# Performance work log

Measured on AMD Instinct MI355X. Metric: run time of the kernel, lower is better.

Reference implementation:

```python
import jax, jax.numpy as jnp
import numpy as np

N_NODES = 100000
N_EDGES = 1200000
D_IN = 16
D_EDGE = 4
H = 64


def setup_inputs() -> dict:
    key = jax.random.key(0)
    ks = jax.random.split(key, 20)
    s = 0.05
    inp = {
        "src": jax.random.randint(ks[0], (N_EDGES,), 0, N_NODES),
        "dst": jax.random.randint(ks[1], (N_EDGES,), 0, N_NODES),
        "t": jax.random.uniform(ks[2], (N_EDGES,), dtype=jnp.float32),
        "x": jax.random.normal(ks[3], (N_NODES, D_IN), dtype=jnp.float32),
        "edge_attr": jax.random.normal(ks[4], (N_EDGES, D_EDGE), dtype=jnp.float32),
        # x_encoder
        "Wx": jax.random.normal(ks[5], (D_IN, H), dtype=jnp.float32) * s,
        "bx": jnp.zeros((H,), dtype=jnp.float32),
        # TransformerConv (heads=1, concat=False)
        "Wq": jax.random.normal(ks[6], (H, H), dtype=jnp.float32) * s,
        "bq": jnp.zeros((H,), dtype=jnp.float32),
        "Wk": jax.random.normal(ks[7], (H, H), dtype=jnp.float32) * s,
        "bk": jnp.zeros((H,), dtype=jnp.float32),
        "Wv": jax.random.normal(ks[8], (H, H), dtype=jnp.float32) * s,
        "bv": jnp.zeros((H,), dtype=jnp.float32),
        "We": jax.random.normal(ks[9], (D_EDGE, H), dtype=jnp.float32) * s,  # lin_edge, bias=False
        "Ws": jax.random.normal(ks[10], (H, H), dtype=jnp.float32) * s,  # lin_skip (root weight)
        "bs": jnp.zeros((H,), dtype=jnp.float32),
        # MLP head
        "W1": jax.random.normal(ks[11], (H, 8), dtype=jnp.float32) * s,
        "b1": jnp.zeros((8,), dtype=jnp.float32),
        "W2": jax.random.normal(ks[12], (8, 1), dtype=jnp.float32) * s,
        "b2": jnp.zeros((1,), dtype=jnp.float32),
    }
    return inp


def reference(src, dst, t, x, edge_attr, Wx, bx, Wq, bq, Wk, bk, Wv, bv, We, Ws, bs, W1, b1, W2, b2):
    # eval mode: dropouts are identity; TGN memory.update_state is a pure
    # side effect and does not influence the returned output.
    xe = x @ Wx + bx                             # [N, H]

    # TransformerConv, heads=1, concat=False, flow src -> dst
    q = xe @ Wq + bq                             # [N, H]
    k = xe @ Wk + bk                             # [N, H]
    v = xe @ Wv + bv                             # [N, H]
    e = edge_attr @ We                           # [E, H]

    k_e = k[src] + e                             # [E, H]
    v_e = v[src] + e                             # [E, H]
    alpha = jnp.sum(q[dst] * k_e, axis=-1) / jnp.sqrt(jnp.float32(H))  # [E]

    # softmax over incoming edges per destination node
    m = jax.ops.segment_max(alpha, dst, num_segments=N_NODES)
    a = jnp.exp(alpha - m[dst])
    denom = jax.ops.segment_sum(a, dst, num_segments=N_NODES)
    w = a / (denom[dst] + 1e-16)                 # [E]

    agg = jax.ops.segment_sum(v_e * w[:, None], dst, num_segments=N_NODES)  # [N, H]
    h_local = agg + (xe @ Ws + bs)               # root/skip connection

    h = h_local[dst]                             # [E, H]
    h = jax.nn.relu(h @ W1 + b1)                 # [E, 8]
    out = (h @ W2 + b2)[:, 0]                    # [E]
    return out
```

## Files before the change

kernel.cpp:

```cpp
#include <hip/hip_runtime.h>

#define H 64
#define CAP 48

typedef int nint4 __attribute__((ext_vector_type(4)));

#define OFF_M   0
#define OFF_U   256
#define OFF_W   272
#define OFF_C   288
#define OFF_R   292
#define OFF_R0  356
#define OFF_PV  360
#define OFF_PE  488
#define OFF_PS  520
#define OFF_BH1 648
#define OFF_BH2 656
#define CST_N   664

__device__ __forceinline__ unsigned f2bf(float f) {
    unsigned u = __float_as_uint(f);
    u += 0x7fffu + ((u >> 16) & 1u);
    return u >> 16;
}
__device__ __forceinline__ float bf_lo(unsigned u) { return __uint_as_float(u << 16); }
__device__ __forceinline__ float bf_hi(unsigned u) { return __uint_as_float(u & 0xffff0000u); }

struct Params {
    const int* src; const int* dst; const float4* ea4; const float* x;
    const float* Wx; const float* bx;
    const float* Wq; const float* bq;
    const float* Wk; const float* bk;
    const float* Wv; const float* bv;
    const float* We; const float* Ws; const float* bs;
    const float* W1; const float* b1; const float* W2; const float* b2;
    int* cursor; nint4* csr; float* cst; float* g; float* out;
    int N, E;
};

__device__ void do_fold(const Params& P, float* __restrict__ cst)
{
    __shared__ float sWf[4][16][64];
    __shared__ float sbf[4][64];
    const int t = threadIdx.x;
    const int c = t & 63, m = t >> 6;
    const float* W; const float* b;
    switch (m) {
        case 0:  W = P.Wq; b = P.bq; break;
        case 1:  W = P.Wk; b = P.bk; break;
        case 2:  W = P.Wv; b = P.bv; break;
        default: W = P.Ws; b = P.bs; break;
    }
    float acc[16];
#pragma unroll
    for (int i = 0; i < 16; ++i) acc[i] = 0.f;
    float bacc = b[c];
    for (int j = 0; j < 64; ++j) {
        const float wv = W[j * 64 + c];
        bacc += P.bx[j] * wv;
#pragma unroll
        for (int i = 0; i < 16; ++i) acc[i] += P.Wx[i * 64 + j] * wv;
    }
#pragma unroll
    for (int i = 0; i < 16; ++i) sWf[m][i][c] = acc[i];
    sbf[m][c] = bacc;
    __syncthreads();

    {
        const int i = t >> 4, j = t & 15;
        float s = 0.f;
        for (int cc = 0; cc < 64; ++cc) s += sWf[0][i][cc] * sWf[1][j][cc];
        cst[OFF_M + i * 16 + j] = s;
    }
    if (t < 16) {
        float su = 0.f, sw = 0.f;
        for (int cc = 0; cc < 64; ++cc) {
            su += sWf[1][t][cc] * sbf[0][cc];
            sw += sWf[0][t][cc] * sbf[1][cc];
        }
        cst[OFF_U + t] = su;
        cst[OFF_W + t] = sw;
    }
    if (t == 0) {
        float s = 0.f;
        for (int cc = 0; cc < 64; ++cc) s += sbf[0][cc] * sbf[1][cc];
        cst[OFF_C] = s;
    }
    if (t < 64) {
        const int j = t >> 4, i = t & 15;
        float s = 0.f;
        for (int cc = 0; cc < 64; ++cc) s += P.We[j * 64 + cc] * sWf[0][i][cc];
        cst[OFF_R + j * 16 + i] = s;
    }
    if (t < 4) {
        float s = 0.f;
        for (int cc = 0; cc < 64; ++cc) s += P.We[t * 64 + cc] * sbf[0][cc];
        cst[OFF_R0 + t] = s;
    }
    if (t < 128) {
        const int i = t >> 3, j = t & 7;
        float sv = 0.f, ss = 0.f;
        for (int cc = 0; cc < 64; ++cc) {
            const float w1 = P.W1[cc * 8 + j];
            sv += sWf[2][i][cc] * w1;
            ss += sWf[3][i][cc] * w1;
        }
        cst[OFF_PV + i * 8 + j] = sv;
        cst[OFF_PS + i * 8 + j] = ss;
    }
    if (t < 32) {
        const int mm = t >> 3, j = t & 7;
        float s = 0.f;
        for (int cc = 0; cc < 64; ++cc) s += P.We[mm * 64 + cc] * P.W1[cc * 8 + j];
        cst[OFF_PE + mm * 8 + j] = s;
    }
    if (t < 8) {
        float s1 = 0.f, s2 = 0.f;
        for (int cc = 0; cc < 64; ++cc) {
            const float w1 = P.W1[cc * 8 + t];
            s1 += sbf[2][cc] * w1;
            s2 += sbf[3][cc] * w1;
        }
        cst[OFF_BH1 + t] = s1;
        cst[OFF_BH2 + t] = s2 + P.b1[t];
    }
}

__global__ __launch_bounds__(256) void k_fill(Params P)
{
    if (blockIdx.x == 0) {
        do_fold(P, P.cst);
        return;
    }
    const int e = (blockIdx.x - 1) * 256 + threadIdx.x;
    if (e >= P.E) return;
    const int s = P.src[e];
    const int d = P.dst[e];
    const float4 A = P.ea4[e];
    const int pos = atomicAdd(&P.cursor[d], 1);
    if (pos < CAP) {
        nint4 ent;
        ent.x = s;
        ent.y = e;
        ent.z = (int)(f2bf(A.x) | (f2bf(A.y) << 16));
        ent.w = (int)(f2bf(A.z) | (f2bf(A.w) << 16));
        P.csr[(size_t)d * CAP + pos] = ent;
    }
}

__global__ __launch_bounds__(128) void k_agg(Params P)
{
    const int t = threadIdx.x;
    const int l = t & 63;
    const int n = blockIdx.x * 2 + (t >> 6);
    if (n >= P.N) return;
    const int grp = l >> 4;
    const int cg_ = l & 15;
    const float* __restrict__ cst = P.cst;

    const int deg = min(P.cursor[n], CAP);
    const size_t nbase = (size_t)n * CAP;

    const float xd = P.x[(size_t)n * 16 + cg_];

    float y = cst[OFF_U + cg_];
#pragma unroll
    for (int i = 0; i < 16; ++i)
        y += __shfl(xd, i) * cst[OFF_M + i * 16 + cg_];

    float pr0 = cst[OFF_R + 0 * 16 + cg_] * xd;
    float pr1 = cst[OFF_R + 1 * 16 + cg_] * xd;
    float pr2 = cst[OFF_R + 2 * 16 + cg_] * xd;
    float pr3 = cst[OFF_R + 3 * 16 + cg_] * xd;
    float pcd = cst[OFF_W + cg_] * xd;
#pragma unroll
    for (int d = 1; d < 16; d <<= 1) {
        pr0 += __shfl_xor(pr0, d);
        pr1 += __shfl_xor(pr1, d);
        pr2 += __shfl_xor(pr2, d);
        pr3 += __shfl_xor(pr3, d);
        pcd += __shfl_xor(pcd, d);
    }
    const float r0 = pr0 + cst[OFF_R0 + 0];
    const float r1 = pr1 + cst[OFF_R0 + 1];
    const float r2 = pr2 + cst[OFF_R0 + 2];
    const float r3 = pr3 + cst[OFF_R0 + 3];
    const float cd = pcd + cst[OFF_C];

    float T = 0.f, S0 = 0.f, S1 = 0.f, S2 = 0.f, S3 = 0.f, den = 0.f;

    for (int base = 0; base < deg; base += 8) {
        const int ia = base + grp;
        const int ib = base + 4 + grp;
        const bool va = ia < deg;
        const bool vb = ib < deg;
        const nint4 Ea = P.csr[nbase + (va ? ia : 0)];
        const nint4 Eb = P.csr[nbase + (vb ? ib : 0)];
        const float xsa = P.x[(size_t)Ea.x * 16 + cg_];
        const float xsb = P.x[(size_t)Eb.x * 16 + cg_];
        {
            const float A0 = bf_lo((unsigned)Ea.z), A1 = bf_hi((unsigned)Ea.z);
            const float A2 = bf_lo((unsigned)Ea.w), A3 = bf_hi((unsigned)Ea.w);
            float p = y * xsa;
            p += __shfl_xor(p, 1);
            p += __shfl_xor(p, 2);
            p += __shfl_xor(p, 4);
            p += __shfl_xor(p, 8);
            p += cd + A0 * r0 + A1 * r1 + A2 * r2 + A3 * r3;
            const float a = va ? __expf(p * 0.125f) : 0.f;
            T += a * xsa;
            S0 += a * A0; S1 += a * A1; S2 += a * A2; S3 += a * A3;
            den += a;
        }
        {
            const float A0 = bf_lo((unsigned)Eb.z), A1 = bf_hi((unsigned)Eb.z);
            const float A2 = bf_lo((unsigned)Eb.w), A3 = bf_hi((unsigned)Eb.w);
            float p = y * xsb;
            p += __shfl_xor(p, 1);
            p += __shfl_xor(p, 2);
            p += __shfl_xor(p, 4);
            p += __shfl_xor(p, 8);
            p += cd + A0 * r0 + A1 * r1 + A2 * r2 + A3 * r3;
            const float a = vb ? __expf(p * 0.125f) : 0.f;
            T += a * xsb;
            S0 += a * A0; S1 += a * A1; S2 += a * A2; S3 += a * A3;
            den += a;
        }
    }

    T   += __shfl_xor(T, 16);   T   += __shfl_xor(T, 32);
    den += __shfl_xor(den, 16); den += __shfl_xor(den, 32);
    S0  += __shfl_xor(S0, 16);  S0  += __shfl_xor(S0, 32);
    S1  += __shfl_xor(S1, 16);  S1  += __shfl_xor(S1, 32);
    S2  += __shfl_xor(S2, 16);  S2  += __shfl_xor(S2, 32);
    S3  += __shfl_xor(S3, 16);  S3  += __shfl_xor(S3, 32);

    const float inv = 1.f / (den + 1e-16f);
    const float Ti = T * inv;

    float hp[8];
#pragma unroll
    for (int j = 0; j < 8; ++j)
        hp[j] = Ti * cst[OFF_PV + cg_ * 8 + j] + xd * cst[OFF_PS + cg_ * 8 + j];
#pragma unroll
    for (int j = 0; j < 8; ++j) {
        hp[j] += __shfl_xor(hp[j], 1);
        hp[j] += __shfl_xor(hp[j], 2);
        hp[j] += __shfl_xor(hp[j], 4);
        hp[j] += __shfl_xor(hp[j], 8);
    }
    const float dinv = den * inv;
    float val = P.b2[0];
#pragma unroll
    for (int j = 0; j < 8; ++j) {
        const float hid = hp[j]
            + inv * (S0 * cst[OFF_PE + 0 * 8 + j] + S1 * cst[OFF_PE + 1 * 8 + j]
                   + S2 * cst[OFF_PE + 2 * 8 + j] + S3 * cst[OFF_PE + 3 * 8 + j])
            + dinv * cst[OFF_BH1 + j] + cst[OFF_BH2 + j];
        val += fmaxf(hid, 0.f) * P.W2[j];
    }

    if (l == 0) P.g[n] = val;
}

__global__ __launch_bounds__(256) void k_out(
    const int* __restrict__ dst, const float* __restrict__ g,
    float* __restrict__ out, int E)
{
    const int e = blockIdx.x * 256 + threadIdx.x;
    if (e < E) out[e] = g[dst[e]];
}

extern "C" void kernel_launch(void* const* d_in, const int* in_sizes, int n_in,
                              void* d_out, int out_size, void* d_ws, size_t ws_size,
                              hipStream_t stream)
{
    Params P;
    P.src = (const int*)d_in[0];
    P.dst = (const int*)d_in[1];
    P.x   = (const float*)d_in[3];
    P.ea4 = (const float4*)d_in[4];
    P.Wx  = (const float*)d_in[5];
    P.bx  = (const float*)d_in[6];
    P.Wq  = (const float*)d_in[7];
    P.bq  = (const float*)d_in[8];
    P.Wk  = (const float*)d_in[9];
    P.bk  = (const float*)d_in[10];
    P.Wv  = (const float*)d_in[11];
    P.bv  = (const float*)d_in[12];
    P.We  = (const float*)d_in[13];
    P.Ws  = (const float*)d_in[14];
    P.bs  = (const float*)d_in[15];
    P.W1  = (const float*)d_in[16];
    P.b1  = (const float*)d_in[17];
    P.W2  = (const float*)d_in[18];
    P.b2  = (const float*)d_in[19];

    P.E = in_sizes[0];
    P.N = in_sizes[3] / 16;
    P.out = (float*)d_out;

    P.csr    = (nint4*)d_ws;
    P.cursor = (int*)(P.csr + (size_t)P.N * CAP);
    P.cst    = (float*)(P.cursor + P.N);
    P.g      = P.cst + CST_N;

    hipMemsetAsync(P.cursor, 0, (size_t)P.N * sizeof(int), stream);

    const int nbE = (P.E + 255) / 256;
    k_fill<<<nbE + 1, 256, 0, stream>>>(P);
    k_agg<<<(P.N + 1) / 2, 128, 0, stream>>>(P);
    k_out<<<nbE, 256, 0, stream>>>(P.dst, P.g, P.out, P.E);
}
```

Before: 292.0 us.

## Map one node per 16-lane group in aggregation and precompute per-node projections

```diff
diff --git a/kernel.cpp b/kernel.cpp
--- a/kernel.cpp
+++ b/kernel.cpp
@@ -1,6 +1,5 @@
 #include <hip/hip_runtime.h>
 
-#define H 64
 #define CAP 48
 
 typedef int nint4 __attribute__((ext_vector_type(4)));
@@ -34,7 +33,8 @@
     const float* Wv; const float* bv;
     const float* We; const float* Ws; const float* bs;
     const float* W1; const float* b1; const float* W2; const float* b2;
-    int* cursor; nint4* csr; float* cst; float* g; float* out;
+    int* cursor; nint4* csr; float* cst;
+    float* yv; float* rv; float* cdv; float* g; float* out;
     int N, E;
 };
 
@@ -126,25 +126,65 @@
     }
 }
 
+__global__ __launch_bounds__(256) void k_init(Params P)
+{
+    if (blockIdx.x == 0) { do_fold(P, P.cst); return; }
+    const int i = (blockIdx.x - 1) * 256 + threadIdx.x;
+    if (i < P.N) P.cursor[i] = 0;
+}
+
 __global__ __launch_bounds__(256) void k_fill(Params P)
 {
-    if (blockIdx.x == 0) {
-        do_fold(P, P.cst);
+    const int t = threadIdx.x;
+    const int nbE = (P.E + 255) >> 8;
+    if ((int)blockIdx.x < nbE) {
+        const int e = blockIdx.x * 256 + t;
+        if (e >= P.E) return;
+        const int s = P.src[e];
+        const int d = P.dst[e];
+        const float4 A = P.ea4[e];
+        const int pos = atomicAdd(&P.cursor[d], 1);
+        if (pos < CAP) {
+            nint4 ent;
+            ent.x = s;
+            ent.y = e;
+            ent.z = (int)(f2bf(A.x) | (f2bf(A.y) << 16));
+            ent.w = (int)(f2bf(A.z) | (f2bf(A.w) << 16));
+            P.csr[(size_t)d * CAP + pos] = ent;
+        }
         return;
     }
-    const int e = (blockIdx.x - 1) * 256 + threadIdx.x;
-    if (e >= P.E) return;
-    const int s = P.src[e];
-    const int d = P.dst[e];
-    const float4 A = P.ea4[e];
-    const int pos = atomicAdd(&P.cursor[d], 1);
-    if (pos < CAP) {
-        nint4 ent;
-        ent.x = s;
-        ent.y = e;
-        ent.z = (int)(f2bf(A.x) | (f2bf(A.y) << 16));
-        ent.w = (int)(f2bf(A.z) | (f2bf(A.w) << 16));
-        P.csr[(size_t)d * CAP + pos] = ent;
+
+    __shared__ float sx[16][16];
+    const float* __restrict__ cst = P.cst;
+    const int node0 = ((int)blockIdx.x - nbE) * 16;
+    const int nl = t >> 4, cg = t & 15;
+    {
+        const int idx = node0 * 16 + t;
+        sx[nl][cg] = (idx < P.N * 16) ? P.x[idx] : 0.f;
+    }
+    __syncthreads();
+    const int n = node0 + nl;
+    if (n >= P.N) return;
+
+    float y = cst[OFF_U + cg];
+#pragma unroll
+    for (int i = 0; i < 16; ++i)
+        y += sx[nl][i] * cst[OFF_M + i * 16 + cg];
+    P.yv[(size_t)n * 16 + cg] = y;
+
+    if (cg < 4) {
+        float r = cst[OFF_R0 + cg];
+#pragma unroll
+        for (int i = 0; i < 16; ++i)
+            r += cst[OFF_R + cg * 16 + i] * sx[nl][i];
+        P.rv[(size_t)n * 4 + cg] = r;
+    } else if (cg == 4) {
+        float cd = cst[OFF_C];
+#pragma unroll
+        for (int i = 0; i < 16; ++i)
+            cd += cst[OFF_W + i] * sx[nl][i];
+        P.cdv[n] = cd;
     }
 }
 
@@ -152,52 +192,37 @@
 {
     const int t = threadIdx.x;
     const int l = t & 63;
-    const int n = blockIdx.x * 2 + (t >> 6);
-    if (n >= P.N) return;
+    const int wv = t >> 6;
     const int grp = l >> 4;
-    const int cg_ = l & 15;
+    const int cg  = l & 15;
+    const int n   = (blockIdx.x * 2 + wv) * 4 + grp;
     const float* __restrict__ cst = P.cst;
 
-    const int deg = min(P.cursor[n], CAP);
-    const size_t nbase = (size_t)n * CAP;
-
-    const float xd = P.x[(size_t)n * 16 + cg_];
-
-    float y = cst[OFF_U + cg_];
-#pragma unroll
-    for (int i = 0; i < 16; ++i)
-        y += __shfl(xd, i) * cst[OFF_M + i * 16 + cg_];
-
-    float pr0 = cst[OFF_R + 0 * 16 + cg_] * xd;
-    float pr1 = cst[OFF_R + 1 * 16 + cg_] * xd;
-    float pr2 = cst[OFF_R + 2 * 16 + cg_] * xd;
-    float pr3 = cst[OFF_R + 3 * 16 + cg_] * xd;
-    float pcd = cst[OFF_W + cg_] * xd;
-#pragma unroll
-    for (int d = 1; d < 16; d <<= 1) {
-        pr0 += __shfl_xor(pr0, d);
-        pr1 += __shfl_xor(pr1, d);
-        pr2 += __shfl_xor(pr2, d);
-        pr3 += __shfl_xor(pr3, d);
-        pcd += __shfl_xor(pcd, d);
-    }
-    const float r0 = pr0 + cst[OFF_R0 + 0];
-    const float r1 = pr1 + cst[OFF_R0 + 1];
-    const float r2 = pr2 + cst[OFF_R0 + 2];
-    const float r3 = pr3 + cst[OFF_R0 + 3];
-    const float cd = pcd + cst[OFF_C];
+    const bool vn = n < P.N;
+    const int nn = vn ? n : P.N - 1;
+    const int deg = vn ? min(P.cursor[nn], CAP) : 0;
+    const size_t nbase = (size_t)nn * CAP;
+
+    const float xd = P.x[(size_t)nn * 16 + cg];
+    const float y  = P.yv[(size_t)nn * 16 + cg];
+    const float4 rv = *(const float4*)&P.rv[(size_t)nn * 4];
+    const float cd = P.cdv[nn];
+
+    int degM = deg;
+    degM = max(degM, __shfl_xor(degM, 16));
+    degM = max(degM, __shfl_xor(degM, 32));
 
     float T = 0.f, S0 = 0.f, S1 = 0.f, S2 = 0.f, S3 = 0.f, den = 0.f;
 
-    for (int base = 0; base < deg; base += 8) {
-        const int ia = base + grp;
-        const int ib = base + 4 + grp;
-        const bool va = ia < deg;
-        const bool vb = ib < deg;
-        const nint4 Ea = P.csr[nbase + (va ? ia : 0)];
-        const nint4 Eb = P.csr[nbase + (vb ? ib : 0)];
-        const float xsa = P.x[(size_t)Ea.x * 16 + cg_];
-        const float xsb = P.x[(size_t)Eb.x * 16 + cg_];
+    for (int i = 0; i < degM; i += 2) {
+        const bool va = i < deg;
+        const bool vb = (i + 1) < deg;
+        const nint4 Ea = P.csr[nbase + (va ? i : 0)];
+        const nint4 Eb = P.csr[nbase + (vb ? i + 1 : 0)];
+        const int sa = va ? Ea.x : 0;
+        const int sb = vb ? Eb.x : 0;
+        const float xsa = P.x[(size_t)sa * 16 + cg];
+        const float xsb = P.x[(size_t)sb * 16 + cg];
         {
             const float A0 = bf_lo((unsigned)Ea.z), A1 = bf_hi((unsigned)Ea.z);
             const float A2 = bf_lo((unsigned)Ea.w), A3 = bf_hi((unsigned)Ea.w);
@@ -206,7 +231,7 @@
             p += __shfl_xor(p, 2);
             p += __shfl_xor(p, 4);
             p += __shfl_xor(p, 8);
-            p += cd + A0 * r0 + A1 * r1 + A2 * r2 + A3 * r3;
+            p += cd + A0 * rv.x + A1 * rv.y + A2 * rv.z + A3 * rv.w;
             const float a = va ? __expf(p * 0.125f) : 0.f;
             T += a * xsa;
             S0 += a * A0; S1 += a * A1; S2 += a * A2; S3 += a * A3;
@@ -220,7 +245,7 @@
             p += __shfl_xor(p, 2);
             p += __shfl_xor(p, 4);
             p += __shfl_xor(p, 8);
-            p += cd + A0 * r0 + A1 * r1 + A2 * r2 + A3 * r3;
+            p += cd + A0 * rv.x + A1 * rv.y + A2 * rv.z + A3 * rv.w;
             const float a = vb ? __expf(p * 0.125f) : 0.f;
             T += a * xsb;
             S0 += a * A0; S1 += a * A1; S2 += a * A2; S3 += a * A3;
@@ -228,20 +253,13 @@
         }
     }
 
-    T   += __shfl_xor(T, 16);   T   += __shfl_xor(T, 32);
-    den += __shfl_xor(den, 16); den += __shfl_xor(den, 32);
-    S0  += __shfl_xor(S0, 16);  S0  += __shfl_xor(S0, 32);
-    S1  += __shfl_xor(S1, 16);  S1  += __shfl_xor(S1, 32);
-    S2  += __shfl_xor(S2, 16);  S2  += __shfl_xor(S2, 32);
-    S3  += __shfl_xor(S3, 16);  S3  += __shfl_xor(S3, 32);
-
     const float inv = 1.f / (den + 1e-16f);
     const float Ti = T * inv;
 
     float hp[8];
 #pragma unroll
     for (int j = 0; j < 8; ++j)
-        hp[j] = Ti * cst[OFF_PV + cg_ * 8 + j] + xd * cst[OFF_PS + cg_ * 8 + j];
+        hp[j] = Ti * cst[OFF_PV + cg * 8 + j] + xd * cst[OFF_PS + cg * 8 + j];
 #pragma unroll
     for (int j = 0; j < 8; ++j) {
         hp[j] += __shfl_xor(hp[j], 1);
@@ -260,7 +278,7 @@
         val += fmaxf(hid, 0.f) * P.W2[j];
     }
 
-    if (l == 0) P.g[n] = val;
+    if (cg == 0 && vn) P.g[n] = val;
 }
 
 __global__ __launch_bounds__(256) void k_out(
@@ -303,12 +321,16 @@
     P.csr    = (nint4*)d_ws;
     P.cursor = (int*)(P.csr + (size_t)P.N * CAP);
     P.cst    = (float*)(P.cursor + P.N);
-    P.g      = P.cst + CST_N;
-
-    hipMemsetAsync(P.cursor, 0, (size_t)P.N * sizeof(int), stream);
+    P.yv     = P.cst + CST_N;
+    P.rv     = P.yv + (size_t)P.N * 16;
+    P.cdv    = P.rv + (size_t)P.N * 4;
+    P.g      = P.cdv + P.N;
 
     const int nbE = (P.E + 255) / 256;
-    k_fill<<<nbE + 1, 256, 0, stream>>>(P);
-    k_agg<<<(P.N + 1) / 2, 128, 0, stream>>>(P);
+    const int nbN16 = (P.N + 15) / 16;
+
+    k_init<<<1 + (P.N + 255) / 256, 256, 0, stream>>>(P);
+    k_fill<<<nbE + nbN16, 256, 0, stream>>>(P);
+    k_agg<<<(P.N + 7) / 8, 128, 0, stream>>>(P);
     k_out<<<nbE, 256, 0, stream>>>(P.dst, P.g, P.out, P.E);
 }
```

Result: faster. 259.2 us (-11.2%).
